# Optimization experiments

Measured on AMD Instinct MI355X. Metric: run time of the kernel, lower is better.

The kernel has to match this reference:

```python
import jax, jax.numpy as jnp
import numpy as np
from jax import lax

E = 4; D_MODEL = 128; D_FF = 128; DT_RANK = 32; D_STATE = 16
L = 12; PAD = 12  # padding_factor=1.0 -> pad L extra zeros
K_TOP = 6; U = 1e-6; EPS = 1e-5
BATCH = 8; NODES = 307; BN = BATCH * NODES
FREQ_IN = (L + PAD) // 2 + 1 + K_TOP  # 19
FREQ_OUT = L // 2 + 1                 # 7


def setup_inputs() -> dict:
    key = jax.random.key(0)
    ks = jax.random.split(key, 14)
    x = jax.random.normal(ks[0], (BN, L, D_MODEL), jnp.float32)
    graph = jax.random.normal(ks[1], (BATCH, L, D_FF, D_FF), jnp.float32) * (1.0 / D_FF)
    in_w = jax.random.normal(ks[2], (E, 2 * D_FF, D_MODEL), jnp.float32) * 0.05
    in_b = jax.random.normal(ks[3], (E, 2 * D_FF), jnp.float32) * 0.02
    x_w = jax.random.normal(ks[4], (E, DT_RANK + 2 * D_STATE + D_FF, D_FF), jnp.float32) * 0.05
    dt_w = jax.random.uniform(ks[5], (E, D_FF, DT_RANK), jnp.float32,
                              -(DT_RANK ** -0.5), DT_RANK ** -0.5)
    dt_b = -2.0 + 0.1 * jax.random.normal(ks[6], (E, D_FF), jnp.float32)
    A_log = jnp.broadcast_to(jnp.log(jnp.arange(1, D_STATE + 1, dtype=jnp.float32))[None, None, :],
                             (E, 1, D_STATE))
    out_w = jax.random.normal(ks[7], (E, D_MODEL, D_FF), jnp.float32) * 0.05
    out_b = jax.random.normal(ks[8], (E, D_MODEL), jnp.float32) * 0.02
    fw_r = jax.random.normal(ks[9], (E, FREQ_OUT, FREQ_IN), jnp.float32) * (FREQ_IN ** -0.5)
    fw_i = jax.random.normal(ks[10], (E, FREQ_OUT, FREQ_IN), jnp.float32) * (FREQ_IN ** -0.5)
    norm_w = jnp.ones((E, D_MODEL), jnp.float32)
    blk_w = jnp.full((E,), 0.5, jnp.float32)
    blk_b = jnp.full((E,), 0.5, jnp.float32)
    return dict(x=x, graph=graph, in_w=in_w, in_b=in_b, x_w=x_w, dt_w=dt_w, dt_b=dt_b,
                A_log=A_log, out_w=out_w, out_b=out_b, fw_r=fw_r, fw_i=fw_i,
                norm_w=norm_w, blk_w=blk_w, blk_b=blk_b)


def _rmsnorm(x, w):
    return x * lax.rsqrt(jnp.mean(x * x, axis=-1, keepdims=True) + EPS) * w


def _mamba_block(x, graph, in_w, in_b, x_w, dt_w, dt_b, A_log, out_w, out_b, fw_r, fw_i):
    bn, Ls, d = x.shape
    # --- FFT frequency gating ---
    x_padded = jnp.concatenate([x, jnp.zeros((bn, PAD, d), x.dtype)], axis=1)
    fp = jnp.fft.rfft(x_padded, axis=1)          # [bn, 13, d] complex
    f = jnp.fft.rfft(x, axis=1)                  # [bn, 7, d] complex
    sq_adj = (f.real + U) ** 2 + (f.imag + U) ** 2
    fs = -jnp.sort(-sq_adj, axis=1)[:, :K_TOP]   # top-K along freq dim, descending
    cat = jnp.concatenate([fp, fs.astype(fp.dtype)], axis=1)  # [bn, 19, d]
    W = lax.complex(fw_r, fw_i)                  # [7, 19]
    freq_proj = jnp.einsum('bkd,ok->bod', cat, W)  # [bn, 7, d]
    wf = jax.nn.softmax(freq_proj.real ** 2 + freq_proj.imag ** 2, axis=2)
    x_freq = jnp.fft.irfft(wf * f, axis=1)       # [bn, 12, d] (n = 2*(7-1))
    # --- input projection ---
    xz = x @ in_w.T + in_b
    xs, z = jnp.split(xz, 2, axis=-1)
    xs = jax.nn.silu(xs)
    # --- SSM ---
    A = -jnp.exp(A_log.astype(jnp.float32))      # [1, d_state]
    dbcd = xs @ x_w.T
    delta, B, C, Dp = jnp.split(dbcd, [DT_RANK, DT_RANK + D_STATE, DT_RANK + 2 * D_STATE], axis=-1)
    delta = jax.nn.softplus(delta @ dt_w.T + dt_b)  # [bn, L, d_ff]
    # graph mixing over nodes: bn = batch * n
    batch = graph.shape[0]
    delta = delta.reshape(batch, -1, Ls, D_FF)
    delta = jnp.einsum('bnsd,bsda->bnsa', delta, graph).reshape(bn, Ls, D_FF)
    deltaA = jnp.exp(delta[..., None] * A)             # [bn, L, d_ff, d_state]
    BX = delta[..., None] * B[:, :, None, :] * xs[..., None]
    dA_t = jnp.moveaxis(deltaA, 1, 0)
    bx_t = jnp.moveaxis(BX, 1, 0)

    def step(h, ab):
        dA, bx = ab
        h = dA * h + bx
        return h, h

    h0 = jnp.zeros((bn, D_FF, D_STATE), xs.dtype)
    _, hs = lax.scan(step, h0, (dA_t, bx_t))
    hs = jnp.moveaxis(hs, 0, 1)                        # [bn, L, d_ff, d_state]
    y = jnp.einsum('blds,bls->bld', hs, C) + Dp * xs
    # --- gate + output ---
    out = y * jax.nn.silu(z) * x_freq
    return out @ out_w.T + out_b


def reference(x, graph, in_w, in_b, x_w, dt_w, dt_b, A_log, out_w, out_b,
              fw_r, fw_i, norm_w, blk_w, blk_b):
    for i in range(E):
        xn = _rmsnorm(x, norm_w[i])
        out = _mamba_block(xn, graph, in_w[i], in_b[i], x_w[i], dt_w[i], dt_b[i],
                           A_log[i], out_w[i], out_b[i], fw_r[i], fw_i[i])
        out = blk_w[i] * out + blk_b[i]
        x = x + out  # dropout is identity in eval
    return jax.nn.silu(x)
```

## Files before the change

### kernel.cpp

```cpp
#include <hip/hip_runtime.h>
#include <math.h>

#define BN    2456
#define LSEQ  12
#define DM    128
#define NODES 307
#define MROWS 29472
#define FREQ_BLKS  1228
#define FUSED2_BLKS 480

typedef __bf16 bfx8 __attribute__((ext_vector_type(8)));
typedef __bf16 bfx4 __attribute__((ext_vector_type(4)));
typedef float  f32x4 __attribute__((ext_vector_type(4)));

#define MFMA16(a, b, c) __builtin_amdgcn_mfma_f32_16x16x32_bf16(a, b, c, 0, 0, 0)

__device__ __forceinline__ float fsilu(float v)     { return v / (1.0f + __expf(-v)); }
__device__ __forceinline__ float fsoftplus(float x) { return fmaxf(x, 0.f) + __logf(1.0f + __expf(-fabsf(x))); }

__global__ __launch_bounds__(256)
void k_convert(const float* __restrict__ in_w, const float* __restrict__ x_w,
               const float* __restrict__ dt_w, const float* __restrict__ out_w,
               const float* __restrict__ graph,
               const float* __restrict__ fw_r, const float* __restrict__ fw_i,
               __bf16* __restrict__ in_w_sw, __bf16* __restrict__ x_w_sw,
               __bf16* __restrict__ dtw_sw, __bf16* __restrict__ out_w_sw,
               __bf16* __restrict__ graph_sw, float* __restrict__ mw) {
    int idx = blockIdx.x * 256 + threadIdx.x;
    if (idx < 131072) {
        int o = idx;
        int e = o >> 15, r = o & 32767;
        int frag = r >> 9, lane = (r >> 3) & 63, j = r & 7;
        int nt = frag >> 2, kc = frag & 3, lm = lane & 15, lq = lane >> 4;
        in_w_sw[o] = (__bf16)in_w[e * 32768 + (nt * 16 + lm) * 128 + kc * 32 + lq * 8 + j];
        return;
    }
    idx -= 131072;
    if (idx < 98304) {
        int o = idx;
        int e = o / 24576, r = o - e * 24576;
        int frag = r >> 9, lane = (r >> 3) & 63, j = r & 7;
        int nt = frag >> 2, kc = frag & 3, lm = lane & 15, lq = lane >> 4;
        x_w_sw[o] = (__bf16)x_w[e * 24576 + (nt * 16 + lm) * 128 + kc * 32 + lq * 8 + j];
        return;
    }
    idx -= 98304;
    if (idx < 16384) {
        int o = idx;
        int e = o >> 12, r = o & 4095;
        int nt = r >> 9, lane = (r >> 3) & 63, j = r & 7;
        int lm = lane & 15, lq = lane >> 4;
        dtw_sw[o] = (__bf16)dt_w[e * 4096 + (nt * 16 + lm) * 32 + lq * 8 + j];
        return;
    }
    idx -= 16384;
    if (idx < 65536) {
        int o = idx;
        int e = o >> 14, r = o & 16383;
        int frag = r >> 9, lane = (r >> 3) & 63, j = r & 7;
        int f = frag >> 2, kc = frag & 3, lm = lane & 15, lq = lane >> 4;
        out_w_sw[o] = (__bf16)out_w[e * 16384 + (f * 16 + lm) * 128 + kc * 32 + lq * 8 + j];
        return;
    }
    idx -= 65536;
    if (idx < 1572864) {
        int bl = idx >> 14, r = idx & 16383;
        int dd = r >> 7, a = r & 127;
        int nt = a >> 4, lm = a & 15, kc = dd >> 5, lq = (dd >> 3) & 3, j = dd & 7;
        graph_sw[(size_t)bl * 16384 + ((size_t)((nt * 4 + kc) * 64 + lq * 16 + lm)) * 8 + j] =
            (__bf16)graph[(size_t)bl * 16384 + dd * 128 + a];
        return;
    }
    idx -= 1572864;
    if (idx < 336) {
        int o = idx;
        int e = o / 84, r = o - e * 84;
        int o2 = r / 12, l = r - o2 * 12;
        float mr = 0.f, mi = 0.f;
        for (int k = 0; k < 13; ++k) {
            float sv, cv;
            __sincosf(6.283185307179586f * (float)(k * l) / 24.0f, &sv, &cv);
            const float wr = fw_r[e * 133 + o2 * 19 + k], wi = fw_i[e * 133 + o2 * 19 + k];
            mr += wr * cv + wi * sv;
            mi += wi * cv - wr * sv;
        }
        mw[e * 256 + (o2 * 12 + l) * 2]     = mr;
        mw[e * 256 + (o2 * 12 + l) * 2 + 1] = mi;
        return;
    }
    idx -= 336;
    if (idx < 168) {
        int o = idx;
        int e = o / 42, r = o - e * 42;
        int o2 = r / 6, k = r - o2 * 6;
        mw[e * 256 + 168 + (o2 * 6 + k) * 2]     = fw_r[e * 133 + o2 * 19 + 13 + k];
        mw[e * 256 + 168 + (o2 * 6 + k) * 2 + 1] = fw_i[e * 133 + o2 * 19 + 13 + k];
    }
}

__global__ __launch_bounds__(256)
void k_fused(const float* __restrict__ xcur, const float* __restrict__ norm_w,
             const __bf16* __restrict__ WiSw, const float* __restrict__ in_b,
             const __bf16* __restrict__ WxSw, const __bf16* __restrict__ DWSw,
             const float* __restrict__ dt_b, const __bf16* __restrict__ GSw,
             const float* __restrict__ mw,
             __bf16* __restrict__ scanp, float* __restrict__ bcf32,
             __bf16* __restrict__ xfq_bf, int e) {
    const int tid = threadIdx.x;

    if (blockIdx.x < FREQ_BLKS) {
        __shared__ float sred2[2][2][12];
        const int hh = tid >> 7, t7 = tid & 127;
        const int lane = tid & 63, w2 = (tid >> 6) & 1;
        const int row = blockIdx.x * 2 + hh;
        const int b = row / NODES, n = row - b * NODES;

        constexpr float SQ32 = 0.8660254037844386f;
        constexpr float C12[12] = {1.f, SQ32, 0.5f, 0.f, -0.5f, -SQ32, -1.f, -SQ32, -0.5f, 0.f, 0.5f, SQ32};
        constexpr float S12[12] = {0.f, 0.5f, SQ32, 1.f, SQ32, 0.5f, 0.f, -0.5f, -SQ32, -1.f, -SQ32, -0.5f};

        const float* xp = xcur + (size_t)row * 1536 + t7;
        float xv[12], v[12];
#pragma unroll
        for (int l = 0; l < 12; ++l) { xv[l] = xp[l * 128]; v[l] = xv[l] * xv[l]; }
#pragma unroll
        for (int off = 32; off; off >>= 1)
#pragma unroll
            for (int i = 0; i < 12; ++i) v[i] += __shfl_xor(v[i], off, 64);
        if (lane == 0) {
#pragma unroll
            for (int i = 0; i < 12; ++i) sred2[hh][w2][i] = v[i];
        }
        __syncthreads();
#pragma unroll
        for (int i = 0; i < 12; ++i) v[i] = sred2[hh][0][i] + sred2[hh][1][i];
        __syncthreads();

        const float nrmw = norm_w[e * DM + t7];
        float xnr[12];
#pragma unroll
        for (int l = 0; l < 12; ++l)
            xnr[l] = xv[l] * rsqrtf(v[l] * (1.0f / 128.0f) + 1e-5f) * nrmw;

        float fr[7], fi[7];
#pragma unroll
        for (int o2 = 0; o2 < 7; ++o2) {
            float r = 0.f, im = 0.f;
#pragma unroll
            for (int l = 0; l < 12; ++l) {
                const int t = (o2 * l) % 12;
                r += xnr[l] * C12[t];
                im -= xnr[l] * S12[t];
            }
            fr[o2] = r; fi[o2] = im;
        }

        float a7[7];
#pragma unroll
        for (int o2 = 0; o2 < 7; ++o2) {
            const float ar = fr[o2] + 1e-6f, ai = fi[o2] + 1e-6f;
            a7[o2] = ar * ar + ai * ai;
        }
#pragma unroll
        for (int pss = 0; pss < 6; ++pss)
#pragma unroll
            for (int j = 0; j < 6; ++j) {
                const float hi = fmaxf(a7[j], a7[j + 1]);
                const float lo = fminf(a7[j], a7[j + 1]);
                a7[j] = hi; a7[j + 1] = lo;
            }

        const float* Me = mw + e * 256;
        float p7[7];
#pragma unroll
        for (int o2 = 0; o2 < 7; ++o2) {
            float pr = 0.f, pi = 0.f;
#pragma unroll
            for (int l = 0; l < 12; ++l) {
                pr += xnr[l] * Me[(o2 * 12 + l) * 2];
                pi += xnr[l] * Me[(o2 * 12 + l) * 2 + 1];
            }
#pragma unroll
            for (int k = 0; k < 6; ++k) {
                pr += a7[k] * Me[168 + (o2 * 6 + k) * 2];
                pi += a7[k] * Me[168 + (o2 * 6 + k) * 2 + 1];
            }
            p7[o2] = pr * pr + pi * pi;
        }

        float m7[7];
#pragma unroll
        for (int i = 0; i < 7; ++i) m7[i] = p7[i];
#pragma unroll
        for (int off = 32; off; off >>= 1)
#pragma unroll
            for (int i = 0; i < 7; ++i) m7[i] = fmaxf(m7[i], __shfl_xor(m7[i], off, 64));
        if (lane == 0) {
#pragma unroll
            for (int i = 0; i < 7; ++i) sred2[hh][w2][i] = m7[i];
        }
        __syncthreads();
#pragma unroll
        for (int i = 0; i < 7; ++i) m7[i] = fmaxf(sred2[hh][0][i], sred2[hh][1][i]);
        __syncthreads();

        float ex[7], sm[7];
#pragma unroll
        for (int i = 0; i < 7; ++i) { ex[i] = __expf(p7[i] - m7[i]); sm[i] = ex[i]; }
#pragma unroll
        for (int off = 32; off; off >>= 1)
#pragma unroll
            for (int i = 0; i < 7; ++i) sm[i] += __shfl_xor(sm[i], off, 64);
        if (lane == 0) {
#pragma unroll
            for (int i = 0; i < 7; ++i) sred2[hh][w2][i] = sm[i];
        }
        __syncthreads();
#pragma unroll
        for (int i = 0; i < 7; ++i) sm[i] = sred2[hh][0][i] + sred2[hh][1][i];

        float gr[7], gi[7];
#pragma unroll
        for (int o2 = 0; o2 < 7; ++o2) {
            const float wf = ex[o2] / sm[o2];
            gr[o2] = wf * fr[o2];
            gi[o2] = wf * fi[o2];
        }

        const size_t xb = ((size_t)(b * 12) * NODES + n) * 128 + t7;
#pragma unroll
        for (int l = 0; l < 12; ++l) {
            float val = gr[0] + ((l & 1) ? -gr[6] : gr[6]);
#pragma unroll
            for (int o2 = 1; o2 < 6; ++o2) {
                const int t = (o2 * l) % 12;
                val += 2.0f * (gr[o2] * C12[t] - gi[o2] * S12[t]);
            }
            xfq_bf[xb + (size_t)l * (NODES * 128)] = (__bf16)(val * (1.0f / 12.0f));
        }
        return;
    }

    __shared__ __bf16 sxs[4 * 16 * 136];
    __shared__ __bf16 sdelta[4 * 16 * 136];
    __shared__ __bf16 sdel32[4 * 16 * 40];

    const int fid = blockIdx.x - FREQ_BLKS;
    const int bl = fid / 5;
    const int n0 = (fid - bl * 5) * 64;
    const int wave = tid >> 6, lane = tid & 63;
    const int lm = lane & 15, lq = lane >> 4;
    const int b = bl / 12, l = bl - b * 12;
    const int nbase = n0 + wave * 16;
    const size_t rowbase = (size_t)bl * NODES + nbase;
    __bf16* sxsW = sxs + wave * 16 * 136;
    __bf16* sdeltaW = sdelta + wave * 16 * 136;
    __bf16* sdel32W = sdel32 + wave * 16 * 40;

    const int ng = min(nbase + lm, NODES - 1);
    const float* xrow = xcur + ((size_t)(b * NODES + ng) * 12 + l) * 128 + lq * 8;
    float xv[4][8];
#pragma unroll
    for (int kc = 0; kc < 4; ++kc) {
        float4 p0 = *(const float4*)(xrow + kc * 32);
        float4 p1 = *(const float4*)(xrow + kc * 32 + 4);
        xv[kc][0] = p0.x; xv[kc][1] = p0.y; xv[kc][2] = p0.z; xv[kc][3] = p0.w;
        xv[kc][4] = p1.x; xv[kc][5] = p1.y; xv[kc][6] = p1.z; xv[kc][7] = p1.w;
    }
    float ss = 0.f;
#pragma unroll
    for (int kc = 0; kc < 4; ++kc)
#pragma unroll
        for (int j = 0; j < 8; ++j) ss += xv[kc][j] * xv[kc][j];
    ss += __shfl_xor(ss, 16, 64);
    ss += __shfl_xor(ss, 32, 64);
    const float rms = rsqrtf(ss * (1.0f / 128.0f) + 1e-5f);

    bfx8 af[4];
    const float* nwp = norm_w + e * DM + lq * 8;
#pragma unroll
    for (int kc = 0; kc < 4; ++kc) {
        float4 w0 = *(const float4*)(nwp + kc * 32);
        float4 w1 = *(const float4*)(nwp + kc * 32 + 4);
        af[kc][0] = (__bf16)(xv[kc][0] * rms * w0.x);
        af[kc][1] = (__bf16)(xv[kc][1] * rms * w0.y);
        af[kc][2] = (__bf16)(xv[kc][2] * rms * w0.z);
        af[kc][3] = (__bf16)(xv[kc][3] * rms * w0.w);
        af[kc][4] = (__bf16)(xv[kc][4] * rms * w1.x);
        af[kc][5] = (__bf16)(xv[kc][5] * rms * w1.y);
        af[kc][6] = (__bf16)(xv[kc][6] * rms * w1.z);
        af[kc][7] = (__bf16)(xv[kc][7] * rms * w1.w);
    }

    const __bf16* WiP = WiSw + (size_t)e * 32768;
    const f32x4 z4 = {0.f, 0.f, 0.f, 0.f};

    {
        f32x4 acc8[8];
#pragma unroll
        for (int ntl = 0; ntl < 8; ++ntl) acc8[ntl] = z4;
#pragma unroll
        for (int ntl = 0; ntl < 8; ++ntl)
#pragma unroll
            for (int kc = 0; kc < 4; ++kc) {
                bfx8 bb = *(const bfx8*)(WiP + ((ntl * 4 + kc) * 64 + lane) * 8);
                acc8[ntl] = MFMA16(af[kc], bb, acc8[ntl]);
            }
#pragma unroll
        for (int ntl = 0; ntl < 8; ++ntl) {
            const int col = ntl * 16 + lm;
            const float bias = in_b[e * 256 + col];
#pragma unroll
            for (int r = 0; r < 4; ++r) {
                const int nl = lq * 4 + r;
                const float v = fsilu(acc8[ntl][r] + bias);
                sxsW[nl * 136 + col] = (__bf16)v;
                if (nbase + nl < NODES)
                    scanp[(rowbase + nl) * 512 + col * 4 + 1] = (__bf16)v;
            }
        }
    }
    {
        f32x4 acc8[8];
#pragma unroll
        for (int ntl = 0; ntl < 8; ++ntl) acc8[ntl] = z4;
#pragma unroll
        for (int ntl = 0; ntl < 8; ++ntl)
#pragma unroll
            for (int kc = 0; kc < 4; ++kc) {
                bfx8 bb = *(const bfx8*)(WiP + (((ntl + 8) * 4 + kc) * 64 + lane) * 8);
                acc8[ntl] = MFMA16(af[kc], bb, acc8[ntl]);
            }
#pragma unroll
        for (int ntl = 0; ntl < 8; ++ntl) {
            const int col = (ntl + 8) * 16 + lm;
            const float bias = in_b[e * 256 + col];
#pragma unroll
            for (int r = 0; r < 4; ++r) {
                const int nl = lq * 4 + r;
                const float v = fsilu(acc8[ntl][r] + bias);
                if (nbase + nl < NODES)
                    scanp[(rowbase + nl) * 512 + (col - 128) * 4 + 3] = (__bf16)v;
            }
        }
    }
    __syncthreads();

    {
        bfx8 ax[4];
#pragma unroll
        for (int kc = 0; kc < 4; ++kc)
            ax[kc] = *(const bfx8*)(sxsW + lm * 136 + kc * 32 + lq * 8);

        const __bf16* WxP = WxSw + (size_t)e * 24576;
        f32x4 acc12[12];
#pragma unroll
        for (int ntl = 0; ntl < 12; ++ntl) acc12[ntl] = z4;
#pragma unroll
        for (int ntl = 0; ntl < 12; ++ntl)
#pragma unroll
            for (int kc = 0; kc < 4; ++kc) {
                bfx8 bb = *(const bfx8*)(WxP + ((ntl * 4 + kc) * 64 + lane) * 8);
                acc12[ntl] = MFMA16(ax[kc], bb, acc12[ntl]);
            }
#pragma unroll
        for (int ntl = 0; ntl < 12; ++ntl) {
            const int col = ntl * 16 + lm;
#pragma unroll
            for (int r = 0; r < 4; ++r) {
                const int nl = lq * 4 + r;
                const float v = acc12[ntl][r];
                const int ok = (nbase + nl) < NODES;
                if (col < 32) sdel32W[nl * 40 + col] = (__bf16)v;
                else if (col < 64) { if (ok) bcf32[(rowbase + nl) * 32 + (col - 32)] = v; }
                else if (ok) scanp[(rowbase + nl) * 512 + (col - 64) * 4 + 2] = (__bf16)v;
            }
        }
    }
    __syncthreads();

    {
        bfx8 ad = *(const bfx8*)(sdel32W + lm * 40 + lq * 8);
        const __bf16* DWp = DWSw + (size_t)e * 4096;
#pragma unroll
        for (int ntl = 0; ntl < 8; ++ntl) {
            bfx8 bb = *(const bfx8*)(DWp + (ntl * 64 + lane) * 8);
            f32x4 dacc = MFMA16(ad, bb, z4);
            const int col = ntl * 16 + lm;
            const float bias = dt_b[e * 128 + col];
#pragma unroll
            for (int r = 0; r < 4; ++r) {
                const int nl = lq * 4 + r;
                sdeltaW[nl * 136 + col] = (__bf16)fsoftplus(dacc[r] + bias);
            }
        }
    }
    __syncthreads();

    {
        bfx8 ag[4];
#pragma unroll
        for (int kc = 0; kc < 4; ++kc)
            ag[kc] = *(const bfx8*)(sdeltaW + lm * 136 + kc * 32 + lq * 8);

        const __bf16* Gp = GSw + (size_t)bl * 16384;
#pragma unroll
        for (int ntl = 0; ntl < 8; ++ntl) {
            f32x4 gacc = z4;
#pragma unroll
            for (int kc = 0; kc < 4; ++kc) {
                bfx8 bb = *(const bfx8*)(Gp + ((ntl * 4 + kc) * 64 + lane) * 8);
                gacc = MFMA16(ag[kc], bb, gacc);
            }
            const int col = ntl * 16 + lm;
#pragma unroll
            for (int r = 0; r < 4; ++r) {
                const int nl = lq * 4 + r;
                if (nbase + nl < NODES)
                    scanp[(rowbase + nl) * 512 + col * 4 + 0] = (__bf16)gacc[r];
            }
        }
    }
}

__global__ __launch_bounds__(128)
void k_scanout(const float* __restrict__ xcur, const __bf16* __restrict__ scanp,
               const float* __restrict__ bcf32, const __bf16* __restrict__ xfq_bf,
               const float* __restrict__ A_log, const __bf16* __restrict__ WoSw,
               const float* __restrict__ out_b, const float* __restrict__ blk_w,
               const float* __restrict__ blk_b, float* __restrict__ xout, int e, int last) {
    __shared__ __bf16 s_out[16 * 136];
    const int row = blockIdx.x, tid = threadIdx.x;
    const int b = row / NODES, n = row - b * NODES;

    constexpr float LOGT[16] = {0.f, 0.6931472f, 1.0986123f, 1.3862944f, 1.6094379f, 1.7917595f,
                                1.9459101f, 2.0794415f, 2.1972246f, 2.3025851f, 2.3978953f,
                                2.4849066f, 2.5649494f, 2.6390573f, 2.7080502f, 2.7725887f};

    bfx4 sc12[12];
    const size_t sb = ((size_t)(b * 12) * NODES + n) * 512 + (size_t)tid * 4;
#pragma unroll
    for (int l = 0; l < 12; ++l)
        sc12[l] = *(const bfx4*)(scanp + sb + (size_t)l * (NODES * 512));

    __bf16 xq[12];
    const size_t xb = ((size_t)(b * 12) * NODES + n) * 128 + tid;
#pragma unroll
    for (int l = 0; l < 12; ++l)
        xq[l] = xfq_bf[xb + (size_t)l * (NODES * 128)];

    int chainOK = 1;
#pragma unroll
    for (int s = 0; s < 16; ++s)
        chainOK &= (fabsf(A_log[e * 16 + s] - LOGT[s]) < 1e-4f) ? 1 : 0;

#pragma unroll
    for (int r = 12; r < 16; ++r) s_out[r * 136 + tid] = (__bf16)0.f;

    float h[16];
#pragma unroll
    for (int j = 0; j < 16; ++j) h[j] = 0.f;

    if (chainOK) {
        float q1a[12];
#pragma unroll
        for (int l = 0; l < 12; ++l) q1a[l] = __expf(-(float)sc12[l][0]);
#pragma unroll
        for (int l = 0; l < 12; ++l) {
            const float dl = (float)sc12[l][0], xsv = (float)sc12[l][1];
            const float dlx = dl * xsv;
            const float* bc = bcf32 + ((size_t)(b * 12 + l) * NODES + n) * 32;
            const float q1 = q1a[l];
            const float q2 = q1 * q1, q4 = q2 * q2, q8 = q4 * q4;
            float pw[16];
            pw[0] = q1;        pw[1] = q2;        pw[2] = q1 * q2;    pw[3] = q4;
            pw[4] = q1 * q4;   pw[5] = q2 * q4;   pw[6] = pw[2] * q4; pw[7] = q8;
            pw[8] = q1 * q8;   pw[9] = q2 * q8;   pw[10] = pw[2] * q8; pw[11] = q4 * q8;
            pw[12] = pw[4] * q8; pw[13] = pw[5] * q8; pw[14] = pw[6] * q8; pw[15] = q8 * q8;
            float y0 = 0.f, y1 = 0.f, y2 = 0.f, y3 = 0.f;
#pragma unroll
            for (int j = 0; j < 4; ++j) {
                h[j]      = pw[j]      * h[j]      + bc[j]      * dlx;  y0 += h[j]      * bc[16 + j];
                h[j + 4]  = pw[j + 4]  * h[j + 4]  + bc[j + 4]  * dlx;  y1 += h[j + 4]  * bc[20 + j];
                h[j + 8]  = pw[j + 8]  * h[j + 8]  + bc[j + 8]  * dlx;  y2 += h[j + 8]  * bc[24 + j];
                h[j + 12] = pw[j + 12] * h[j + 12] + bc[j + 12] * dlx;  y3 += h[j + 12] * bc[28 + j];
            }
            float y = (y0 + y1) + (y2 + y3);
            y += (float)sc12[l][2] * xsv;
            const float g = y * (float)sc12[l][3] * (float)xq[l];
            s_out[l * 136 + tid] = (__bf16)g;
        }
    } else {
        float As[16];
#pragma unroll
        for (int s = 0; s < 16; ++s) As[s] = -__expf(A_log[e * 16 + s]);
#pragma unroll
        for (int l = 0; l < 12; ++l) {
            const float dl = (float)sc12[l][0], xsv = (float)sc12[l][1];
            const float dlx = dl * xsv;
            const float* bc = bcf32 + ((size_t)(b * 12 + l) * NODES + n) * 32;
            float y = 0.f;
#pragma unroll
            for (int j = 0; j < 16; ++j) {
                const float a = __expf(dl * As[j]);
                h[j] = a * h[j] + bc[j] * dlx;
                y += h[j] * bc[16 + j];
            }
            y += (float)sc12[l][2] * xsv;
            const float g = y * (float)sc12[l][3] * (float)xq[l];
            s_out[l * 136 + tid] = (__bf16)g;
        }
    }
    __syncthreads();

    const int wave = tid >> 6, lane = tid & 63;
    const int lm = lane & 15, lq = lane >> 4;
    const __bf16* Wop = WoSw + (size_t)e * 16384;
    bfx8 a[4];
#pragma unroll
    for (int kc = 0; kc < 4; ++kc)
        a[kc] = *(const bfx8*)(s_out + lm * 136 + kc * 32 + lq * 8);

    f32x4 acc[4];
#pragma unroll
    for (int nt = 0; nt < 4; ++nt) acc[nt] = (f32x4){0.f, 0.f, 0.f, 0.f};
#pragma unroll
    for (int nt = 0; nt < 4; ++nt) {
        const int f = wave * 4 + nt;
#pragma unroll
        for (int kc = 0; kc < 4; ++kc) {
            bfx8 bb = *(const bfx8*)(Wop + ((f * 4 + kc) * 64 + lane) * 8);
            acc[nt] = MFMA16(a[kc], bb, acc[nt]);
        }
    }

    const float bw = blk_w[e], bb2 = blk_b[e];
#pragma unroll
    for (int nt = 0; nt < 4; ++nt) {
        const int col = wave * 64 + nt * 16 + lm;
        const float ob = out_b[e * 128 + col];
#pragma unroll
        for (int r = 0; r < 4; ++r) {
            const int m = lq * 4 + r;
            if (m < 12) {
                const size_t gi = (size_t)row * 1536 + m * 128 + col;
                float vv = bw * (acc[nt][r] + ob) + bb2 + xcur[gi];
                if (last) vv = fsilu(vv);
                xout[gi] = vv;
            }
        }
    }
}

extern "C" void kernel_launch(void* const* d_in, const int* in_sizes, int n_in,
                              void* d_out, int out_size, void* d_ws, size_t ws_size,
                              hipStream_t stream) {
    (void)in_sizes; (void)n_in; (void)out_size; (void)ws_size;
    const float* x_in   = (const float*)d_in[0];
    const float* graph  = (const float*)d_in[1];
    const float* in_w   = (const float*)d_in[2];
    const float* in_b   = (const float*)d_in[3];
    const float* x_w    = (const float*)d_in[4];
    const float* dt_w   = (const float*)d_in[5];
    const float* dt_b   = (const float*)d_in[6];
    const float* A_log  = (const float*)d_in[7];
    const float* out_w  = (const float*)d_in[8];
    const float* out_b  = (const float*)d_in[9];
    const float* fw_r   = (const float*)d_in[10];
    const float* fw_i   = (const float*)d_in[11];
    const float* norm_w = (const float*)d_in[12];
    const float* blk_w  = (const float*)d_in[13];
    const float* blk_b  = (const float*)d_in[14];
    float* out = (float*)d_out;

    float* ws = (float*)d_ws;
    size_t o = 0;
    __bf16* in_w_sw  = (__bf16*)(ws + o); o += 131072 / 2;
    __bf16* x_w_sw   = (__bf16*)(ws + o); o += 98304 / 2;
    __bf16* dtw_sw   = (__bf16*)(ws + o); o += 16384 / 2;
    __bf16* out_w_sw = (__bf16*)(ws + o); o += 65536 / 2;
    __bf16* graph_sw = (__bf16*)(ws + o); o += 1572864 / 2;
    const size_t NE = (size_t)MROWS * 128;
    __bf16* scanp    = (__bf16*)(ws + o); o += (size_t)MROWS * 512 / 2;
    __bf16* xfq_bf   = (__bf16*)(ws + o); o += NE / 2;
    float*  bcf32    = ws + o;            o += (size_t)MROWS * 32;
    float*  mw       = ws + o;            o += 1024;

    hipLaunchKernelGGL(k_convert, dim3(7362), dim3(256), 0, stream,
                       in_w, x_w, dt_w, out_w, graph, fw_r, fw_i,
                       in_w_sw, x_w_sw, dtw_sw, out_w_sw, graph_sw, mw);

    for (int e = 0; e < 4; ++e) {
        const float* xcur = (e == 0) ? x_in : (const float*)out;
        const int last = (e == 3) ? 1 : 0;
        hipLaunchKernelGGL(k_fused, dim3(FREQ_BLKS + FUSED2_BLKS), dim3(256), 0, stream,
                           xcur, norm_w, in_w_sw, in_b, x_w_sw, dtw_sw, dt_b, graph_sw,
                           mw, scanp, bcf32, xfq_bf, e);
        hipLaunchKernelGGL(k_scanout, dim3(BN), dim3(128), 0, stream,
                           xcur, scanp, bcf32, xfq_bf, A_log,
                           out_w_sw, out_b, blk_w, blk_b, out, e, last);
    }
}
```

Measured before the change: 429.8 us.

## Split interleaved scan params into planar arrays, reorder blocks, trim shared memory and barriers

```diff
diff --git a/kernel.cpp b/kernel.cpp
--- a/kernel.cpp
+++ b/kernel.cpp
@@ -10,7 +10,6 @@
 #define FUSED2_BLKS 480
 
 typedef __bf16 bfx8 __attribute__((ext_vector_type(8)));
-typedef __bf16 bfx4 __attribute__((ext_vector_type(4)));
 typedef float  f32x4 __attribute__((ext_vector_type(4)));
 
 #define MFMA16(a, b, c) __builtin_amdgcn_mfma_f32_16x16x32_bf16(a, b, c, 0, 0, 0)
@@ -104,15 +103,18 @@
              const __bf16* __restrict__ WxSw, const __bf16* __restrict__ DWSw,
              const float* __restrict__ dt_b, const __bf16* __restrict__ GSw,
              const float* __restrict__ mw,
-             __bf16* __restrict__ scanp, float* __restrict__ bcf32,
-             __bf16* __restrict__ xfq_bf, int e) {
+             __bf16* __restrict__ dmix_bf, __bf16* __restrict__ xs_bf,
+             __bf16* __restrict__ dpf, __bf16* __restrict__ sz_bf,
+             float* __restrict__ bcf32, __bf16* __restrict__ xfq_bf, int e) {
     const int tid = threadIdx.x;
-
-    if (blockIdx.x < FREQ_BLKS) {
-        __shared__ float sred2[2][2][12];
+    __shared__ __bf16 sxs[4 * 16 * 136];
+    __shared__ __bf16 sdel32[4 * 16 * 40];
+
+    if (blockIdx.x >= FUSED2_BLKS) {
+        float (*sred2)[2][12] = (float (*)[2][12])sxs;
         const int hh = tid >> 7, t7 = tid & 127;
         const int lane = tid & 63, w2 = (tid >> 6) & 1;
-        const int row = blockIdx.x * 2 + hh;
+        const int row = (blockIdx.x - FUSED2_BLKS) * 2 + hh;
         const int b = row / NODES, n = row - b * NODES;
 
         constexpr float SQ32 = 0.8660254037844386f;
@@ -241,11 +243,7 @@
         return;
     }
 
-    __shared__ __bf16 sxs[4 * 16 * 136];
-    __shared__ __bf16 sdelta[4 * 16 * 136];
-    __shared__ __bf16 sdel32[4 * 16 * 40];
-
-    const int fid = blockIdx.x - FREQ_BLKS;
+    const int fid = blockIdx.x;
     const int bl = fid / 5;
     const int n0 = (fid - bl * 5) * 64;
     const int wave = tid >> 6, lane = tid & 63;
@@ -254,7 +252,6 @@
     const int nbase = n0 + wave * 16;
     const size_t rowbase = (size_t)bl * NODES + nbase;
     __bf16* sxsW = sxs + wave * 16 * 136;
-    __bf16* sdeltaW = sdelta + wave * 16 * 136;
     __bf16* sdel32W = sdel32 + wave * 16 * 40;
 
     const int ng = min(nbase + lm, NODES - 1);
@@ -316,7 +313,7 @@
                 const float v = fsilu(acc8[ntl][r] + bias);
                 sxsW[nl * 136 + col] = (__bf16)v;
                 if (nbase + nl < NODES)
-                    scanp[(rowbase + nl) * 512 + col * 4 + 1] = (__bf16)v;
+                    xs_bf[(rowbase + nl) * 128 + col] = (__bf16)v;
             }
         }
     }
@@ -340,11 +337,10 @@
                 const int nl = lq * 4 + r;
                 const float v = fsilu(acc8[ntl][r] + bias);
                 if (nbase + nl < NODES)
-                    scanp[(rowbase + nl) * 512 + (col - 128) * 4 + 3] = (__bf16)v;
-            }
-        }
-    }
-    __syncthreads();
+                    sz_bf[(rowbase + nl) * 128 + (col - 128)] = (__bf16)v;
+            }
+        }
+    }
 
     {
         bfx8 ax[4];
@@ -373,11 +369,10 @@
                 const int ok = (nbase + nl) < NODES;
                 if (col < 32) sdel32W[nl * 40 + col] = (__bf16)v;
                 else if (col < 64) { if (ok) bcf32[(rowbase + nl) * 32 + (col - 32)] = v; }
-                else if (ok) scanp[(rowbase + nl) * 512 + (col - 64) * 4 + 2] = (__bf16)v;
-            }
-        }
-    }
-    __syncthreads();
+                else if (ok) dpf[(rowbase + nl) * 128 + (col - 64)] = (__bf16)v;
+            }
+        }
+    }
 
     {
         bfx8 ad = *(const bfx8*)(sdel32W + lm * 40 + lq * 8);
@@ -391,17 +386,16 @@
 #pragma unroll
             for (int r = 0; r < 4; ++r) {
                 const int nl = lq * 4 + r;
-                sdeltaW[nl * 136 + col] = (__bf16)fsoftplus(dacc[r] + bias);
-            }
-        }
-    }
-    __syncthreads();
+                sxsW[nl * 136 + col] = (__bf16)fsoftplus(dacc[r] + bias);
+            }
+        }
+    }
 
     {
         bfx8 ag[4];
 #pragma unroll
         for (int kc = 0; kc < 4; ++kc)
-            ag[kc] = *(const bfx8*)(sdeltaW + lm * 136 + kc * 32 + lq * 8);
+            ag[kc] = *(const bfx8*)(sxsW + lm * 136 + kc * 32 + lq * 8);
 
         const __bf16* Gp = GSw + (size_t)bl * 16384;
 #pragma unroll
@@ -417,18 +411,20 @@
             for (int r = 0; r < 4; ++r) {
                 const int nl = lq * 4 + r;
                 if (nbase + nl < NODES)
-                    scanp[(rowbase + nl) * 512 + col * 4 + 0] = (__bf16)gacc[r];
+                    dmix_bf[(rowbase + nl) * 128 + col] = (__bf16)gacc[r];
             }
         }
     }
 }
 
 __global__ __launch_bounds__(128)
-void k_scanout(const float* __restrict__ xcur, const __bf16* __restrict__ scanp,
-               const float* __restrict__ bcf32, const __bf16* __restrict__ xfq_bf,
-               const float* __restrict__ A_log, const __bf16* __restrict__ WoSw,
-               const float* __restrict__ out_b, const float* __restrict__ blk_w,
-               const float* __restrict__ blk_b, float* __restrict__ xout, int e, int last) {
+void k_scanout(const float* __restrict__ xcur, const __bf16* __restrict__ dmix_bf,
+               const __bf16* __restrict__ xs_bf, const __bf16* __restrict__ dpf,
+               const __bf16* __restrict__ sz_bf, const float* __restrict__ bcf32,
+               const __bf16* __restrict__ xfq_bf, const float* __restrict__ A_log,
+               const __bf16* __restrict__ WoSw, const float* __restrict__ out_b,
+               const float* __restrict__ blk_w, const float* __restrict__ blk_b,
+               float* __restrict__ xout, int e, int last) {
     __shared__ __bf16 s_out[16 * 136];
     const int row = blockIdx.x, tid = threadIdx.x;
     const int b = row / NODES, n = row - b * NODES;
@@ -437,17 +433,17 @@
                                 1.9459101f, 2.0794415f, 2.1972246f, 2.3025851f, 2.3978953f,
                                 2.4849066f, 2.5649494f, 2.6390573f, 2.7080502f, 2.7725887f};
 
-    bfx4 sc12[12];
-    const size_t sb = ((size_t)(b * 12) * NODES + n) * 512 + (size_t)tid * 4;
-#pragma unroll
-    for (int l = 0; l < 12; ++l)
-        sc12[l] = *(const bfx4*)(scanp + sb + (size_t)l * (NODES * 512));
-
-    __bf16 xq[12];
-    const size_t xb = ((size_t)(b * 12) * NODES + n) * 128 + tid;
-#pragma unroll
-    for (int l = 0; l < 12; ++l)
-        xq[l] = xfq_bf[xb + (size_t)l * (NODES * 128)];
+    const size_t pb = ((size_t)(b * 12) * NODES + n) * 128 + tid;
+    const size_t ps = (size_t)NODES * 128;
+    __bf16 dmx[12], xss[12], dps[12], szs[12], xq[12];
+#pragma unroll
+    for (int l = 0; l < 12; ++l) {
+        dmx[l] = dmix_bf[pb + l * ps];
+        xss[l] = xs_bf[pb + l * ps];
+        dps[l] = dpf[pb + l * ps];
+        szs[l] = sz_bf[pb + l * ps];
+        xq[l]  = xfq_bf[pb + l * ps];
+    }
 
     int chainOK = 1;
 #pragma unroll
@@ -464,10 +460,10 @@
     if (chainOK) {
         float q1a[12];
 #pragma unroll
-        for (int l = 0; l < 12; ++l) q1a[l] = __expf(-(float)sc12[l][0]);
+        for (int l = 0; l < 12; ++l) q1a[l] = __expf(-(float)dmx[l]);
 #pragma unroll
         for (int l = 0; l < 12; ++l) {
-            const float dl = (float)sc12[l][0], xsv = (float)sc12[l][1];
+            const float dl = (float)dmx[l], xsv = (float)xss[l];
             const float dlx = dl * xsv;
             const float* bc = bcf32 + ((size_t)(b * 12 + l) * NODES + n) * 32;
             const float q1 = q1a[l];
@@ -486,8 +482,8 @@
                 h[j + 12] = pw[j + 12] * h[j + 12] + bc[j + 12] * dlx;  y3 += h[j + 12] * bc[28 + j];
             }
             float y = (y0 + y1) + (y2 + y3);
-            y += (float)sc12[l][2] * xsv;
-            const float g = y * (float)sc12[l][3] * (float)xq[l];
+            y += (float)dps[l] * xsv;
+            const float g = y * (float)szs[l] * (float)xq[l];
             s_out[l * 136 + tid] = (__bf16)g;
         }
     } else {
@@ -496,7 +492,7 @@
         for (int s = 0; s < 16; ++s) As[s] = -__expf(A_log[e * 16 + s]);
 #pragma unroll
         for (int l = 0; l < 12; ++l) {
-            const float dl = (float)sc12[l][0], xsv = (float)sc12[l][1];
+            const float dl = (float)dmx[l], xsv = (float)xss[l];
             const float dlx = dl * xsv;
             const float* bc = bcf32 + ((size_t)(b * 12 + l) * NODES + n) * 32;
             float y = 0.f;
@@ -506,8 +502,8 @@
                 h[j] = a * h[j] + bc[j] * dlx;
                 y += h[j] * bc[16 + j];
             }
-            y += (float)sc12[l][2] * xsv;
-            const float g = y * (float)sc12[l][3] * (float)xq[l];
+            y += (float)dps[l] * xsv;
+            const float g = y * (float)szs[l] * (float)xq[l];
             s_out[l * 136 + tid] = (__bf16)g;
         }
     }
@@ -581,7 +577,10 @@
     __bf16* out_w_sw = (__bf16*)(ws + o); o += 65536 / 2;
     __bf16* graph_sw = (__bf16*)(ws + o); o += 1572864 / 2;
     const size_t NE = (size_t)MROWS * 128;
-    __bf16* scanp    = (__bf16*)(ws + o); o += (size_t)MROWS * 512 / 2;
+    __bf16* dmix_bf  = (__bf16*)(ws + o); o += NE / 2;
+    __bf16* xs_bf    = (__bf16*)(ws + o); o += NE / 2;
+    __bf16* dpf      = (__bf16*)(ws + o); o += NE / 2;
+    __bf16* sz_bf    = (__bf16*)(ws + o); o += NE / 2;
     __bf16* xfq_bf   = (__bf16*)(ws + o); o += NE / 2;
     float*  bcf32    = ws + o;            o += (size_t)MROWS * 32;
     float*  mw       = ws + o;            o += 1024;
@@ -593,11 +592,11 @@
     for (int e = 0; e < 4; ++e) {
         const float* xcur = (e == 0) ? x_in : (const float*)out;
         const int last = (e == 3) ? 1 : 0;
-        hipLaunchKernelGGL(k_fused, dim3(FREQ_BLKS + FUSED2_BLKS), dim3(256), 0, stream,
+        hipLaunchKernelGGL(k_fused, dim3(FUSED2_BLKS + FREQ_BLKS), dim3(256), 0, stream,
                            xcur, norm_w, in_w_sw, in_b, x_w_sw, dtw_sw, dt_b, graph_sw,
-                           mw, scanp, bcf32, xfq_bf, e);
+                           mw, dmix_bf, xs_bf, dpf, sz_bf, bcf32, xfq_bf, e);
         hipLaunchKernelGGL(k_scanout, dim3(BN), dim3(128), 0, stream,
-                           xcur, scanp, bcf32, xfq_bf, A_log,
+                           xcur, dmix_bf, xs_bf, dpf, sz_bf, bcf32, xfq_bf, A_log,
                            out_w_sw, out_b, blk_w, blk_b, out, e, last);
     }
 }
```

After: 455.7 us. 1.06x slower.
